# Performance work log

Measured on AMD Instinct MI355X. Metric: run time of the kernel, lower is better.

The kernel has to match this reference:

```python
import jax, jax.numpy as jnp
import numpy as np

BETA = 0.25
K, D = 1024, 64


def setup_inputs() -> dict:
    key = jax.random.key(0)
    k1, k2 = jax.random.split(key)
    z = jax.random.normal(k1, (2, D, 32, 32, 32), dtype=jnp.float32)
    # nn.Embedding initialized uniform(-1/K, 1/K)
    embedding = jax.random.uniform(k2, (K, D), dtype=jnp.float32,
                                   minval=-1.0 / K, maxval=1.0 / K)
    return {"z": z, "embedding": embedding}


def reference(z, embedding):
    # z: [B, D, X, Y, Z] -> [B, X, Y, Z, D]
    zp = jnp.transpose(z, (0, 2, 3, 4, 1))
    latents_shape = zp.shape
    flat = zp.reshape(-1, embedding.shape[1])  # [N, D]

    dist = (jnp.sum(flat ** 2, axis=1, keepdims=True)
            + jnp.sum(embedding ** 2, axis=1)
            - 2.0 * flat @ embedding.T)
    min_encoding_indices = jnp.argmin(dist, axis=1)  # [N]

    z_q = embedding[min_encoding_indices].reshape(latents_shape)

    commitment_loss = jnp.mean((jax.lax.stop_gradient(z_q) - zp) ** 2)
    embedding_loss = jnp.mean((z_q - jax.lax.stop_gradient(zp)) ** 2)
    vq_loss = commitment_loss * BETA + embedding_loss  # point=False branch

    # straight-through estimator
    z_q_st = zp + jax.lax.stop_gradient(z_q - zp)
    out = jnp.transpose(z_q_st, (0, 4, 1, 2, 3))  # back to [B, D, X, Y, Z]
    return out, vq_loss, min_encoding_indices[:, None]
```

## Files before the change

kernel.cpp:

```cpp
#include <hip/hip_runtime.h>
#include <hip/hip_fp16.h>

#define KDIM 1024
#define DDIM 64
#define SPAT 32768
#define NVEC 65536
#define DSP  (DDIM * SPAT)
#define MARGIN 3.0e-4f
#define ZPAD 69
#define QCAP 1536

typedef _Float16 half8 __attribute__((ext_vector_type(8)));
typedef float floatx4 __attribute__((ext_vector_type(4)));

__device__ __forceinline__ float opaque(float x) { asm volatile("" : "+v"(x)); return x; }

__device__ __forceinline__ float np_sumsq64(const float* x) {
    float r8[8];
#pragma unroll
    for (int j = 0; j < 8; ++j) r8[j] = opaque(x[1 + j] * x[1 + j]);
#pragma unroll
    for (int i = 8; i < 56; i += 8) {
#pragma unroll
        for (int j = 0; j < 8; ++j) r8[j] += opaque(x[1 + i + j] * x[1 + i + j]);
    }
    float res = ((r8[0] + r8[1]) + (r8[2] + r8[3])) + ((r8[4] + r8[5]) + (r8[6] + r8[7]));
#pragma unroll
    for (int m = 57; m < 64; ++m) res += opaque(x[m] * x[m]);
    return opaque(x[0] * x[0]) + res;
}

__global__ void vq_prep_e(const float* __restrict__ emb, float* __restrict__ e2,
                          float* __restrict__ h, __half* __restrict__ eh,
                          float* __restrict__ loss) {
    const int tid = threadIdx.x;
    const int kbase = blockIdx.x * 16;
#pragma unroll
    for (int i = 0; i < 4; ++i) {
        int g = i * 256 + tid;
        float v = emb[(size_t)kbase * DDIM + g];
        e2[(size_t)kbase * DDIM + g] = v + v;
        eh[(size_t)kbase * DDIM + g] = (__half)(_Float16)(v * 1024.0f);
    }
    if (tid < 16) h[kbase + tid] = np_sumsq64(emb + (size_t)(kbase + tid) * DDIM);
    if (blockIdx.x == 0 && tid == 0) *loss = 0.f;
}

__global__ __launch_bounds__(256, 4) void vq_mfma_kernel(
    const float* __restrict__ z, const float* __restrict__ emb,
    const __half* __restrict__ eh_, const float* __restrict__ h_,
    const float* __restrict__ e2_, float* __restrict__ out,
    float* __restrict__ loss, float* __restrict__ idxf)
{
    __shared__ float zrow[64 * ZPAD];
    __shared__ float lds_sn[64];
    __shared__ float Lm1[16][64];
    __shared__ float m1f[64];
    __shared__ int   qcnt;
    __shared__ unsigned short      qk[QCAP];
    __shared__ unsigned char       qn[QCAP];
    __shared__ unsigned long long  rbest[64];

    const int tid = threadIdx.x, l = tid & 63, w = tid >> 6;
    const int nbase = blockIdx.x * 64;
    const int b = nbase >> 15, s0 = nbase & (SPAT - 1);
    const int col16 = l & 15, g16 = l >> 4;
    const float* zbase = z + (size_t)b * DSP + s0;

    if (tid == 0) qcnt = 0;
    if (tid < 64) rbest[tid] = ~0ull;

    {
        const int dbase = w * 16;
#pragma unroll
        for (int j = 0; j < 16; ++j)
            zrow[l * ZPAD + dbase + j] = zbase[(size_t)(dbase + j) * SPAT + l];
    }
    __syncthreads();

    if (tid < 64) lds_sn[tid] = np_sumsq64(&zrow[tid * ZPAD]);

    half8 zf[4][2];
#pragma unroll
    for (int nc = 0; nc < 4; ++nc) {
        const int r = nc * 16 + col16;
#pragma unroll
        for (int kp = 0; kp < 2; ++kp) {
            const int d0 = g16 * 8 + kp * 32;
            half8 vh;
#pragma unroll
            for (int u = 0; u < 8; ++u)
                vh[u] = (_Float16)zrow[r * ZPAD + d0 + u];
            zf[nc][kp] = vh;
        }
    }
    __syncthreads();

    float snv[4];
#pragma unroll
    for (int nc = 0; nc < 4; ++nc) snv[nc] = lds_sn[nc * 16 + col16];

    const int myk0 = w * 256;

    float m1[4];
#pragma unroll
    for (int nc = 0; nc < 4; ++nc) m1[nc] = 3.0e38f;
    {
        size_t eoff = (size_t)(myk0 + col16) * DDIM + g16 * 8;
        half8 ef0 = *(const half8*)(eh_ + eoff);
        half8 ef1 = *(const half8*)(eh_ + eoff + 32);
        floatx4 hv = *(const floatx4*)(h_ + myk0 + g16 * 4);
        for (int t = 0; t < 16; ++t) {
            half8 cf0 = ef0, cf1 = ef1; floatx4 chv = hv;
            if (t < 15) {
                const size_t e2off = (size_t)(myk0 + (t + 1) * 16 + col16) * DDIM + g16 * 8;
                ef0 = *(const half8*)(eh_ + e2off);
                ef1 = *(const half8*)(eh_ + e2off + 32);
                hv  = *(const floatx4*)(h_ + myk0 + (t + 1) * 16 + g16 * 4);
            }
#pragma unroll
            for (int nc = 0; nc < 4; ++nc) {
                floatx4 acc = {0.f, 0.f, 0.f, 0.f};
                acc = __builtin_amdgcn_mfma_f32_16x16x32_f16(cf0, zf[nc][0], acc, 0, 0, 0);
                acc = __builtin_amdgcn_mfma_f32_16x16x32_f16(cf1, zf[nc][1], acc, 0, 0, 0);
#pragma unroll
                for (int j = 0; j < 4; ++j) {
                    float dist = fmaf(-0.001953125f, acc[j], snv[nc] + chv[j]);
                    m1[nc] = fminf(m1[nc], dist);
                }
            }
        }
    }
    const int slot = w * 4 + g16;
#pragma unroll
    for (int nc = 0; nc < 4; ++nc) Lm1[slot][nc * 16 + col16] = m1[nc];
    __syncthreads();

    if (tid < 64) {
        float M1 = Lm1[0][tid];
#pragma unroll
        for (int sI = 1; sI < 16; ++sI) M1 = fminf(M1, Lm1[sI][tid]);
        m1f[tid] = M1;
    }
    __syncthreads();

    float thr[4];
#pragma unroll
    for (int nc = 0; nc < 4; ++nc) thr[nc] = m1f[nc * 16 + col16] + MARGIN;
    {
        size_t eoff = (size_t)(myk0 + col16) * DDIM + g16 * 8;
        half8 ef0 = *(const half8*)(eh_ + eoff);
        half8 ef1 = *(const half8*)(eh_ + eoff + 32);
        floatx4 hv = *(const floatx4*)(h_ + myk0 + g16 * 4);
        for (int t = 0; t < 16; ++t) {
            half8 cf0 = ef0, cf1 = ef1; floatx4 chv = hv;
            if (t < 15) {
                const size_t e2off = (size_t)(myk0 + (t + 1) * 16 + col16) * DDIM + g16 * 8;
                ef0 = *(const half8*)(eh_ + e2off);
                ef1 = *(const half8*)(eh_ + e2off + 32);
                hv  = *(const floatx4*)(h_ + myk0 + (t + 1) * 16 + g16 * 4);
            }
            const int rbase = myk0 + t * 16 + g16 * 4;
#pragma unroll
            for (int nc = 0; nc < 4; ++nc) {
                floatx4 acc = {0.f, 0.f, 0.f, 0.f};
                acc = __builtin_amdgcn_mfma_f32_16x16x32_f16(cf0, zf[nc][0], acc, 0, 0, 0);
                acc = __builtin_amdgcn_mfma_f32_16x16x32_f16(cf1, zf[nc][1], acc, 0, 0, 0);
#pragma unroll
                for (int j = 0; j < 4; ++j) {
                    float dist = fmaf(-0.001953125f, acc[j], snv[nc] + chv[j]);
                    if (dist <= thr[nc]) {
                        int p = atomicAdd(&qcnt, 1);
                        if (p < QCAP) {
                            qk[p] = (unsigned short)(rbase + j);
                            qn[p] = (unsigned char)(nc * 16 + col16);
                        }
                    }
                }
            }
        }
    }
    __syncthreads();

    const int qlen = min(qcnt, QCAP);

    for (int i = tid; i < qlen; i += 256) {
        const int k = qk[i], r = qn[i];
        const float* zr = &zrow[r * ZPAD];
        const floatx4* ep = (const floatx4*)(e2_ + (size_t)k * DDIM);
        float acc = 0.f;
#pragma unroll
        for (int dq = 0; dq < 16; ++dq) {
            floatx4 v = ep[dq];
            acc = fmaf(v[0], zr[4 * dq + 0], acc);
            acc = fmaf(v[1], zr[4 * dq + 1], acc);
            acc = fmaf(v[2], zr[4 * dq + 2], acc);
            acc = fmaf(v[3], zr[4 * dq + 3], acc);
        }
        float tt   = lds_sn[r] + h_[k];
        float dist = tt - acc;
        unsigned int db = __float_as_uint(dist);
        atomicMin(&rbest[r], ((unsigned long long)db << 32) | (unsigned int)k);
    }
    __syncthreads();

    if (qcnt > QCAP) {
        const int row = tid & 63, kq = tid >> 6;
        for (int k = kq * 256; k < kq * 256 + 256; ++k) {
            const float* zr = &zrow[row * ZPAD];
            const floatx4* ep = (const floatx4*)(e2_ + (size_t)k * DDIM);
            float acc = 0.f;
#pragma unroll
            for (int dq = 0; dq < 16; ++dq) {
                floatx4 v = ep[dq];
                acc = fmaf(v[0], zr[4 * dq + 0], acc);
                acc = fmaf(v[1], zr[4 * dq + 1], acc);
                acc = fmaf(v[2], zr[4 * dq + 2], acc);
                acc = fmaf(v[3], zr[4 * dq + 3], acc);
            }
            float tt   = lds_sn[row] + h_[k];
            float dist = tt - acc;
            atomicMin(&rbest[row],
                      ((unsigned long long)__float_as_uint(dist) << 32) | (unsigned int)k);
        }
        __syncthreads();
    }

    if (tid < 64) {
        const int I1 = (int)(rbest[tid] & 0xffffffffu);
        const int n = nbase + tid;
        idxf[n] = (float)I1;

        const float* e = emb + (size_t)I1 * DDIM;
        float* op = out + (size_t)b * DSP + s0 + tid;
        float lsum = 0.f;
#pragma unroll
        for (int d = 0; d < DDIM; ++d) {
            float qv = e[d];
            op[(size_t)d * SPAT] = qv;
            float df = qv - zrow[tid * ZPAD + d];
            lsum = fmaf(df, df, lsum);
        }
#pragma unroll
        for (int off = 32; off > 0; off >>= 1)
            lsum += __shfl_down(lsum, off, 64);
        if (tid == 0)
            atomicAdd(loss, lsum * (1.25f / 4194304.0f));
    }
}

extern "C" void kernel_launch(void* const* d_in, const int* in_sizes, int n_in,
                              void* d_out, int out_size, void* d_ws, size_t ws_size,
                              hipStream_t stream) {
    const float* z   = (const float*)d_in[0];
    const float* emb = (const float*)d_in[1];
    float* out  = (float*)d_out;
    float* loss = out + 4194304;
    float* idxf = out + 4194305;

    float* h_  = (float*)d_ws;
    float* e2_ = h_ + KDIM;
    __half* eh_ = (__half*)(e2_ + KDIM * DDIM);

    vq_prep_e<<<KDIM / 16, 256, 0, stream>>>(emb, e2_, h_, eh_, loss);
    vq_mfma_kernel<<<NVEC / 64, 256, 0, stream>>>(z, emb, eh_, h_, e2_, out, loss, idxf);
}
```

Measured before the change: 62.88 us.

## Split codebook search across two blocks with global atomic-min and final kernel

Each 64-vector tile is now handled by two blocks, each scanning half the codebook. Each block keeps its own fp16 prefilter threshold and does its own exact refinement, then merges results through a global 64-bit atomicMin array that is cleared with a memset. A separate kernel reads the winning indices and writes the quantized output, the indices and the loss. The z tile load was changed to a coalesced pattern, the LDS padding and queue capacity were shrunk, and the block-level min reduction now uses LDS atomics. The cost is that z is read three times instead of once, plus an extra memset and an extra kernel launch, in exchange for more blocks and less serial work per block.

New measurement: 84.29 us. 1.34x slower.

```diff
diff --git a/kernel.cpp b/kernel.cpp
--- a/kernel.cpp
+++ b/kernel.cpp
@@ -7,8 +7,8 @@
 #define NVEC 65536
 #define DSP  (DDIM * SPAT)
 #define MARGIN 3.0e-4f
-#define ZPAD 69
-#define QCAP 1536
+#define ZPAD 65
+#define QCAP 768
 
 typedef _Float16 half8 __attribute__((ext_vector_type(8)));
 typedef float floatx4 __attribute__((ext_vector_type(4)));
@@ -47,34 +47,33 @@
 }
 
 __global__ __launch_bounds__(256, 4) void vq_mfma_kernel(
-    const float* __restrict__ z, const float* __restrict__ emb,
-    const __half* __restrict__ eh_, const float* __restrict__ h_,
-    const float* __restrict__ e2_, float* __restrict__ out,
-    float* __restrict__ loss, float* __restrict__ idxf)
+    const float* __restrict__ z, const __half* __restrict__ eh_,
+    const float* __restrict__ h_, const float* __restrict__ e2_,
+    unsigned long long* __restrict__ rbest_g)
 {
     __shared__ float zrow[64 * ZPAD];
     __shared__ float lds_sn[64];
-    __shared__ float Lm1[16][64];
-    __shared__ float m1f[64];
+    __shared__ unsigned int m1bits[64];
     __shared__ int   qcnt;
-    __shared__ unsigned short      qk[QCAP];
-    __shared__ unsigned char       qn[QCAP];
-    __shared__ unsigned long long  rbest[64];
+    __shared__ unsigned short qk[QCAP];
+    __shared__ unsigned char  qn[QCAP];
 
     const int tid = threadIdx.x, l = tid & 63, w = tid >> 6;
-    const int nbase = blockIdx.x * 64;
+    const int ntile = blockIdx.x >> 1, khalf = blockIdx.x & 1;
+    const int koff = khalf * 512;
+    const int nbase = ntile * 64;
     const int b = nbase >> 15, s0 = nbase & (SPAT - 1);
     const int col16 = l & 15, g16 = l >> 4;
     const float* zbase = z + (size_t)b * DSP + s0;
 
     if (tid == 0) qcnt = 0;
-    if (tid < 64) rbest[tid] = ~0ull;
-
-    {
-        const int dbase = w * 16;
-#pragma unroll
-        for (int j = 0; j < 16; ++j)
-            zrow[l * ZPAD + dbase + j] = zbase[(size_t)(dbase + j) * SPAT + l];
+    if (tid < 64) m1bits[tid] = 0xffffffffu;
+
+#pragma unroll
+    for (int j = 0; j < 16; ++j) {
+        const int g = j * 256 + tid;
+        const int d = g >> 6, r = g & 63;
+        zrow[r * ZPAD + d] = zbase[(size_t)d * SPAT + r];
     }
     __syncthreads();
 
@@ -100,7 +99,7 @@
 #pragma unroll
     for (int nc = 0; nc < 4; ++nc) snv[nc] = lds_sn[nc * 16 + col16];
 
-    const int myk0 = w * 256;
+    const int myk0 = koff + w * 128;
 
     float m1[4];
 #pragma unroll
@@ -110,9 +109,9 @@
         half8 ef0 = *(const half8*)(eh_ + eoff);
         half8 ef1 = *(const half8*)(eh_ + eoff + 32);
         floatx4 hv = *(const floatx4*)(h_ + myk0 + g16 * 4);
-        for (int t = 0; t < 16; ++t) {
+        for (int t = 0; t < 8; ++t) {
             half8 cf0 = ef0, cf1 = ef1; floatx4 chv = hv;
-            if (t < 15) {
+            if (t < 7) {
                 const size_t e2off = (size_t)(myk0 + (t + 1) * 16 + col16) * DDIM + g16 * 8;
                 ef0 = *(const half8*)(eh_ + e2off);
                 ef1 = *(const half8*)(eh_ + e2off + 32);
@@ -131,30 +130,22 @@
             }
         }
     }
-    const int slot = w * 4 + g16;
-#pragma unroll
-    for (int nc = 0; nc < 4; ++nc) Lm1[slot][nc * 16 + col16] = m1[nc];
-    __syncthreads();
-
-    if (tid < 64) {
-        float M1 = Lm1[0][tid];
-#pragma unroll
-        for (int sI = 1; sI < 16; ++sI) M1 = fminf(M1, Lm1[sI][tid]);
-        m1f[tid] = M1;
-    }
+#pragma unroll
+    for (int nc = 0; nc < 4; ++nc)
+        atomicMin(&m1bits[nc * 16 + col16], __float_as_uint(m1[nc]));
     __syncthreads();
 
     float thr[4];
 #pragma unroll
-    for (int nc = 0; nc < 4; ++nc) thr[nc] = m1f[nc * 16 + col16] + MARGIN;
+    for (int nc = 0; nc < 4; ++nc) thr[nc] = __uint_as_float(m1bits[nc * 16 + col16]) + MARGIN;
     {
         size_t eoff = (size_t)(myk0 + col16) * DDIM + g16 * 8;
         half8 ef0 = *(const half8*)(eh_ + eoff);
         half8 ef1 = *(const half8*)(eh_ + eoff + 32);
         floatx4 hv = *(const floatx4*)(h_ + myk0 + g16 * 4);
-        for (int t = 0; t < 16; ++t) {
+        for (int t = 0; t < 8; ++t) {
             half8 cf0 = ef0, cf1 = ef1; floatx4 chv = hv;
-            if (t < 15) {
+            if (t < 7) {
                 const size_t e2off = (size_t)(myk0 + (t + 1) * 16 + col16) * DDIM + g16 * 8;
                 ef0 = *(const half8*)(eh_ + e2off);
                 ef1 = *(const half8*)(eh_ + e2off + 32);
@@ -200,13 +191,13 @@
         float tt   = lds_sn[r] + h_[k];
         float dist = tt - acc;
         unsigned int db = __float_as_uint(dist);
-        atomicMin(&rbest[r], ((unsigned long long)db << 32) | (unsigned int)k);
-    }
-    __syncthreads();
+        atomicMin(&rbest_g[nbase + r], ((unsigned long long)db << 32) | (unsigned int)k);
+    }
 
     if (qcnt > QCAP) {
+        __syncthreads();
         const int row = tid & 63, kq = tid >> 6;
-        for (int k = kq * 256; k < kq * 256 + 256; ++k) {
+        for (int k = koff + kq * 128; k < koff + kq * 128 + 128; ++k) {
             const float* zr = &zrow[row * ZPAD];
             const floatx4* ep = (const floatx4*)(e2_ + (size_t)k * DDIM);
             float acc = 0.f;
@@ -220,16 +211,34 @@
             }
             float tt   = lds_sn[row] + h_[k];
             float dist = tt - acc;
-            atomicMin(&rbest[row],
+            atomicMin(&rbest_g[nbase + row],
                       ((unsigned long long)__float_as_uint(dist) << 32) | (unsigned int)k);
         }
-        __syncthreads();
-    }
+    }
+}
+
+__global__ __launch_bounds__(256, 4) void vq_final(
+    const float* __restrict__ z, const float* __restrict__ emb,
+    const unsigned long long* __restrict__ rbest_g, float* __restrict__ out,
+    float* __restrict__ loss, float* __restrict__ idxf)
+{
+    __shared__ float zrow[64 * ZPAD];
+    const int tid = threadIdx.x;
+    const int nbase = blockIdx.x * 64;
+    const int b = nbase >> 15, s0 = nbase & (SPAT - 1);
+    const float* zbase = z + (size_t)b * DSP + s0;
+
+#pragma unroll
+    for (int j = 0; j < 16; ++j) {
+        const int g = j * 256 + tid;
+        const int d = g >> 6, r = g & 63;
+        zrow[r * ZPAD + d] = zbase[(size_t)d * SPAT + r];
+    }
+    __syncthreads();
 
     if (tid < 64) {
-        const int I1 = (int)(rbest[tid] & 0xffffffffu);
-        const int n = nbase + tid;
-        idxf[n] = (float)I1;
+        const int I1 = (int)(rbest_g[nbase + tid] & 0xffffffffu);
+        idxf[nbase + tid] = (float)I1;
 
         const float* e = emb + (size_t)I1 * DDIM;
         float* op = out + (size_t)b * DSP + s0 + tid;
@@ -261,7 +270,11 @@
     float* h_  = (float*)d_ws;
     float* e2_ = h_ + KDIM;
     __half* eh_ = (__half*)(e2_ + KDIM * DDIM);
-
+    unsigned long long* rbest_g =
+        (unsigned long long*)(eh_ + KDIM * DDIM);
+
+    hipMemsetAsync(rbest_g, 0xFF, (size_t)NVEC * 8, stream);
     vq_prep_e<<<KDIM / 16, 256, 0, stream>>>(emb, e2_, h_, eh_, loss);
-    vq_mfma_kernel<<<NVEC / 64, 256, 0, stream>>>(z, emb, eh_, h_, e2_, out, loss, idxf);
-}
+    vq_mfma_kernel<<<NVEC / 32, 256, 0, stream>>>(z, eh_, h_, e2_, rbest_g);
+    vq_final<<<NVEC / 64, 256, 0, stream>>>(z, emb, rbest_g, out, loss, idxf);
+}
```
